# Optimization experiments

Measured on AMD Instinct MI355X. Metric: run time of the kernel, lower is better.

Reference implementation:

```python
import jax, jax.numpy as jnp
import numpy as np

B, S, D, H = 1, 2048, 768, 12
HD = D // H


def layer_norm(x, g, b, eps=1e-5):
    mu = x.mean(-1, keepdims=True)
    var = ((x - mu) ** 2).mean(-1, keepdims=True)
    return (x - mu) * jax.lax.rsqrt(var + eps) * g + b


def setup_inputs() -> dict:
    key = jax.random.key(0)
    ks = jax.random.split(key, 16)
    s = 0.02
    exp_encodings = jax.random.normal(ks[0], (B, S, D), dtype=jnp.float32)
    pert_encodings = jax.random.normal(ks[1], (B, S, D), dtype=jnp.float32)
    adj = (jax.random.uniform(ks[2], (S, S)) < 0.01).astype(jnp.int32)
    adj = adj.at[jnp.arange(S), jnp.arange(S)].set(1)
    in_proj_w = jax.random.normal(ks[3], (3 * D, D)) * s
    in_proj_b = jnp.zeros((3 * D,), jnp.float32)
    out_proj_w = jax.random.normal(ks[4], (D, D)) * s
    out_proj_b = jnp.zeros((D,), jnp.float32)
    ln0_g = jnp.ones((D,), jnp.float32); ln0_b = jnp.zeros((D,), jnp.float32)
    ln1_g = jnp.ones((D,), jnp.float32); ln1_b = jnp.zeros((D,), jnp.float32)
    ln2_g = jnp.ones((D,), jnp.float32); ln2_b = jnp.zeros((D,), jnp.float32)
    w1 = jax.random.normal(ks[5], (D // 2, D)) * s
    b1 = jnp.zeros((D // 2,), jnp.float32)
    w2 = jax.random.normal(ks[6], (D, D // 2)) * s
    b2 = jnp.zeros((D,), jnp.float32)
    return dict(exp_encodings=exp_encodings, pert_encodings=pert_encodings,
                in_proj_w=in_proj_w, in_proj_b=in_proj_b,
                out_proj_w=out_proj_w, out_proj_b=out_proj_b,
                ln0_g=ln0_g, ln0_b=ln0_b, ln1_g=ln1_g, ln1_b=ln1_b,
                ln2_g=ln2_g, ln2_b=ln2_b, w1=w1, b1=b1, w2=w2, b2=b2,
                adj=adj)


def reference(exp_encodings, pert_encodings, in_proj_w, in_proj_b,
              out_proj_w, out_proj_b, ln0_g, ln0_b, ln1_g, ln1_b,
              ln2_g, ln2_b, w1, b1, w2, b2, adj):
    b, s, d = exp_encodings.shape
    hd = d // H
    # additive mask: 0 where edge, -inf elsewhere (diag guaranteed edge)
    mask = jnp.where(adj > 0, 0.0, -jnp.inf).astype(exp_encodings.dtype)
    x_in = layer_norm(exp_encodings + pert_encodings, ln0_g, ln0_b)
    # torch MultiheadAttention (batch_first) self-attention
    qkv = x_in @ in_proj_w.T + in_proj_b          # [b,s,3d]
    q, k, v = jnp.split(qkv, 3, axis=-1)
    q = q.reshape(b, s, H, hd)
    k = k.reshape(b, s, H, hd)
    v = v.reshape(b, s, H, hd)
    scores = jnp.einsum('bqhe,bkhe->bhqk', q, k) / np.sqrt(hd) + mask
    attn = jax.nn.softmax(scores, axis=-1)
    o = jnp.einsum('bhqk,bkhe->bqhe', attn, v).reshape(b, s, d)
    o = o @ out_proj_w.T + out_proj_b
    x = layer_norm(o + x_in, ln1_g, ln1_b)
    ff = jax.nn.relu(x @ w1.T + b1) @ w2.T + b2
    return layer_norm(x + ff, ln2_g, ln2_b)
```

## Files before the change

kernel.cpp:

```cpp
#include <hip/hip_runtime.h>

#define S 2048
#define D 768
#define NH 12
#define HD 64
#define TD (3 * D)

typedef __bf16 bf16_t;
typedef __bf16 v8bf __attribute__((ext_vector_type(8)));
typedef __bf16 v4bf __attribute__((ext_vector_type(4)));
typedef float v4f __attribute__((ext_vector_type(4)));

__device__ __forceinline__ float wave_reduce_sum(float v) {
#pragma unroll
    for (int o = 32; o > 0; o >>= 1) v += __shfl_down(v, o, 64);
    return v;
}
__device__ float block_reduce_sum(float v) {
    __shared__ float t4[4];
    int lane = threadIdx.x & 63, wid = threadIdx.x >> 6;
    v = wave_reduce_sum(v);
    __syncthreads();
    if (lane == 0) t4[wid] = v;
    __syncthreads();
    return t4[0] + t4[1] + t4[2] + t4[3];
}

template <int N>
__device__ __forceinline__ void wait_vmcnt() {
    if constexpr (N == 0) asm volatile("s_waitcnt vmcnt(0)" ::: "memory");
    else if constexpr (N == 1) asm volatile("s_waitcnt vmcnt(1)" ::: "memory");
    else if constexpr (N == 2) asm volatile("s_waitcnt vmcnt(2)" ::: "memory");
    else if constexpr (N == 3) asm volatile("s_waitcnt vmcnt(3)" ::: "memory");
    else if constexpr (N == 4) asm volatile("s_waitcnt vmcnt(4)" ::: "memory");
    else if constexpr (N == 5) asm volatile("s_waitcnt vmcnt(5)" ::: "memory");
    else if constexpr (N == 6) asm volatile("s_waitcnt vmcnt(6)" ::: "memory");
    else if constexpr (N == 7) asm volatile("s_waitcnt vmcnt(7)" ::: "memory");
    else asm volatile("s_waitcnt vmcnt(8)" ::: "memory");
}

#define NW0 (TD * D / 4)
#define NW1 (D * D / 4)
#define NW2 ((D / 2) * D / 4)
#define NW3 (D * (D / 2) / 4)
#define NWALL (NW0 + NW1 + NW2 + NW3)

__global__ __launch_bounds__(256) void addln_cvt(const float* __restrict__ A, const float* __restrict__ Bv,
                                                 const float* __restrict__ g, const float* __restrict__ be,
                                                 bf16_t* __restrict__ out,
                                                 const float* __restrict__ s0, const float* __restrict__ s1,
                                                 const float* __restrict__ s2, const float* __restrict__ s3,
                                                 bf16_t* __restrict__ d0, bf16_t* __restrict__ d1,
                                                 bf16_t* __restrict__ d2, bf16_t* __restrict__ d3) {
    int blk = blockIdx.x, t = threadIdx.x;
    if (blk >= S) {
        int i = (blk - S) * 256 + t;
        const float* sp; bf16_t* dp;
        if (i < NW0) { sp = s0; dp = d0; }
        else if (i < NW0 + NW1) { sp = s1; dp = d1; i -= NW0; }
        else if (i < NW0 + NW1 + NW2) { sp = s2; dp = d2; i -= NW0 + NW1; }
        else if (i < NWALL) { sp = s3; dp = d3; i -= NW0 + NW1 + NW2; }
        else return;
        float4 v = ((const float4*)sp)[i];
        v4bf o = {(bf16_t)v.x, (bf16_t)v.y, (bf16_t)v.z, (bf16_t)v.w};
        *(v4bf*)(dp + (size_t)i * 4) = o;
        return;
    }
    int row = blk;
    const float* a = A + (size_t)row * D;
    const float* b = Bv + (size_t)row * D;
    float x[3];
    float s = 0.f;
#pragma unroll
    for (int i = 0; i < 3; ++i) { int c = t + 256 * i; x[i] = a[c] + b[c]; s += x[i]; }
    float mean = block_reduce_sum(s) * (1.0f / D);
    float vs = 0.f;
#pragma unroll
    for (int i = 0; i < 3; ++i) { float d = x[i] - mean; vs += d * d; }
    float var = block_reduce_sum(vs) * (1.0f / D);
    float rstd = rsqrtf(var + 1e-5f);
#pragma unroll
    for (int i = 0; i < 3; ++i) {
        int c = t + 256 * i;
        out[(size_t)row * D + c] = (bf16_t)((x[i] - mean) * rstd * g[c] + be[c]);
    }
}

template <typename TO>
__global__ __launch_bounds__(256) void ln_only(const bf16_t* __restrict__ X,
                                               const float* __restrict__ g, const float* __restrict__ be,
                                               TO* __restrict__ out) {
    int row = blockIdx.x, t = threadIdx.x;
    const bf16_t* a = X + (size_t)row * D;
    float x[3];
    float s = 0.f;
#pragma unroll
    for (int i = 0; i < 3; ++i) { int c = t + 256 * i; x[i] = (float)a[c]; s += x[i]; }
    float mean = block_reduce_sum(s) * (1.0f / D);
    float vs = 0.f;
#pragma unroll
    for (int i = 0; i < 3; ++i) { float d = x[i] - mean; vs += d * d; }
    float var = block_reduce_sum(vs) * (1.0f / D);
    float rstd = rsqrtf(var + 1e-5f);
#pragma unroll
    for (int i = 0; i < 3; ++i) {
        int c = t + 256 * i;
        out[(size_t)row * D + c] = (TO)((x[i] - mean) * rstd * g[c] + be[c]);
    }
}

#define GBK 64

template <int TM, int TN, int RELU, bool RESID>
__global__ __launch_bounds__(256) void gemm_mfma(const bf16_t* __restrict__ A, const bf16_t* __restrict__ B,
                                                 const float* __restrict__ bias,
                                                 const bf16_t* __restrict__ Rsd, bf16_t* __restrict__ C,
                                                 int M, int N, int K) {
    constexpr int CA = TM * 8;
    constexpr int CHUNKS = (TM + TN) * 8;
    constexpr int P = CHUNKS / 256;
    static_assert(CHUNKS % 256 == 0, "chunk passes must be exact");
    constexpr int MI = TM / 32, NI = TN / 32;
    constexpr int BUFE = (TM + TN) * GBK;
    __shared__ bf16_t smem[2 * BUFE];
    const int t = threadIdx.x;
    const int lane = t & 63, wave = t >> 6;
    const int wr = (wave >> 1) * (TM / 2), wc = (wave & 1) * (TN / 2);
    const int m0 = blockIdx.y * TM, n0 = blockIdx.x * TN;
    const int lm = lane & 15, q = lane >> 4;

    const bf16_t* gp[P];
    int loff[P];
#pragma unroll
    for (int p = 0; p < P; ++p) {
        int c = t + 256 * p;
        if (c < CA) {
            int slab = c / (TM * 4), r4 = c % (TM * 4);
            gp[p] = A + (size_t)(m0 + (r4 >> 2)) * K + slab * 32 + (r4 & 3) * 8;
            loff[p] = slab * (TM * 32) + r4 * 8;
        } else {
            int cc = c - CA;
            int slab = cc / (TN * 4), r4 = cc % (TN * 4);
            gp[p] = B + (size_t)(n0 + (r4 >> 2)) * K + slab * 32 + (r4 & 3) * 8;
            loff[p] = TM * GBK + slab * (TN * 32) + r4 * 8;
        }
    }

    v4f acc[MI][NI] = {};

    auto stage = [&](int buf, int k0) {
#pragma unroll
        for (int p = 0; p < P; ++p)
            __builtin_amdgcn_global_load_lds(
                (const __attribute__((address_space(1))) void*)(gp[p] + k0),
                (__attribute__((address_space(3))) void*)(smem + buf * BUFE + loff[p]), 16, 0, 0);
    };

    stage(0, 0);
    int cur = 0;
    for (int k0 = 0; k0 < K; k0 += GBK) {
        if (k0 + GBK < K) {
            stage(cur ^ 1, k0 + GBK);
            __builtin_amdgcn_sched_barrier(0);
            wait_vmcnt<P>();
        } else {
            __builtin_amdgcn_sched_barrier(0);
            wait_vmcnt<0>();
        }
        __builtin_amdgcn_s_barrier();
        __builtin_amdgcn_sched_barrier(0);

        const bf16_t* As = smem + cur * BUFE;
        const bf16_t* Bs = As + TM * GBK;
        v8bf af[2][MI], bfr[2][NI];
#pragma unroll
        for (int s = 0; s < 2; ++s) {
#pragma unroll
            for (int i = 0; i < MI; ++i)
                af[s][i] = *(const v8bf*)(As + s * (TM * 32) + (wr + i * 16 + lm) * 32 + q * 8);
#pragma unroll
            for (int j = 0; j < NI; ++j)
                bfr[s][j] = *(const v8bf*)(Bs + s * (TN * 32) + (wc + j * 16 + lm) * 32 + q * 8);
        }
#pragma unroll
        for (int s = 0; s < 2; ++s)
#pragma unroll
            for (int i = 0; i < MI; ++i)
#pragma unroll
                for (int j = 0; j < NI; ++j)
                    acc[i][j] = __builtin_amdgcn_mfma_f32_16x16x32_bf16(af[s][i], bfr[s][j], acc[i][j], 0, 0, 0);
        __builtin_amdgcn_sched_barrier(0);
        __builtin_amdgcn_s_barrier();
        cur ^= 1;
    }

#pragma unroll
    for (int i = 0; i < MI; ++i)
#pragma unroll
        for (int j = 0; j < NI; ++j) {
            int col = n0 + wc + j * 16 + lm;
            float bs = bias[col];
#pragma unroll
            for (int r = 0; r < 4; ++r) {
                int row = m0 + wr + i * 16 + q * 4 + r;
                float v = acc[i][j][r] + bs;
                if (RELU) v = fmaxf(v, 0.f);
                if (RESID) v += (float)Rsd[(size_t)row * N + col];
                C[(size_t)row * N + col] = (bf16_t)v;
            }
        }
}

__global__ __launch_bounds__(256) void attn_sparse(const bf16_t* __restrict__ qkv, const int* __restrict__ adj,
                                                   bf16_t* __restrict__ O) {
    __shared__ int s_idx[128];
    __shared__ int s_cnt;
    __shared__ float s_q[D];
    __shared__ float s_p[NH][128];

    const int row = blockIdx.x, t = threadIdx.x;
    const int lane = t & 63, wave = t >> 6;
    if (t == 0) s_cnt = 0;
    __syncthreads();

    const int4* arow = (const int4*)(adj + (size_t)row * S);
#pragma unroll
    for (int p = 0; p < 2; ++p) {
        int4 v = arow[t + 256 * p];
        int base = (t + 256 * p) * 4;
        if (v.x) { int k = atomicAdd(&s_cnt, 1); if (k < 128) s_idx[k] = base + 0; }
        if (v.y) { int k = atomicAdd(&s_cnt, 1); if (k < 128) s_idx[k] = base + 1; }
        if (v.z) { int k = atomicAdd(&s_cnt, 1); if (k < 128) s_idx[k] = base + 2; }
        if (v.w) { int k = atomicAdd(&s_cnt, 1); if (k < 128) s_idx[k] = base + 3; }
    }
    for (int c = t; c < D; c += 256) s_q[c] = (float)qkv[(size_t)row * TD + c];
    __syncthreads();
    const int n = (s_cnt < 128) ? s_cnt : 128;

    for (int it = t; it < n * NH; it += 256) {
        int h = it / n, i = it - h * n;
        int j = s_idx[i];
        const bf16_t* kp = qkv + (size_t)j * TD + D + h * HD;
        const float* qp = s_q + h * HD;
        float dot = 0.f;
#pragma unroll
        for (int c = 0; c < HD; c += 8) {
            v8bf kv = *(const v8bf*)(kp + c);
#pragma unroll
            for (int e = 0; e < 8; ++e) dot += qp[c + e] * (float)kv[e];
        }
        s_p[h][i] = dot * 0.125f;
    }
    __syncthreads();

    for (int h = wave; h < NH; h += 4) {
        float v0 = (lane < n) ? s_p[h][lane] : -1e30f;
        float v1 = (lane + 64 < n) ? s_p[h][lane + 64] : -1e30f;
        float m = fmaxf(v0, v1);
#pragma unroll
        for (int o = 32; o > 0; o >>= 1) m = fmaxf(m, __shfl_xor(m, o, 64));
        float p0 = (lane < n) ? __expf(v0 - m) : 0.f;
        float p1 = (lane + 64 < n) ? __expf(v1 - m) : 0.f;
        float sm = p0 + p1;
#pragma unroll
        for (int o = 32; o > 0; o >>= 1) sm += __shfl_xor(sm, o, 64);
        float inv = 1.f / sm;
        if (lane < n) s_p[h][lane] = p0 * inv;
        if (lane + 64 < n) s_p[h][lane + 64] = p1 * inv;
    }
    __syncthreads();

    for (int o = t; o < D; o += 256) {
        int h = o >> 6, e = o & 63;
        const float* pp = s_p[h];
        float acc = 0.f;
        for (int i = 0; i < n; ++i)
            acc += pp[i] * (float)qkv[(size_t)s_idx[i] * TD + 2 * D + h * HD + e];
        O[(size_t)row * D + o] = (bf16_t)acc;
    }
}

extern "C" void kernel_launch(void* const* d_in, const int* in_sizes, int n_in,
                              void* d_out, int out_size, void* d_ws, size_t ws_size,
                              hipStream_t stream) {
    const float* exp_e = (const float*)d_in[0];
    const float* pert  = (const float*)d_in[1];
    const float* w_in  = (const float*)d_in[2];
    const float* b_in  = (const float*)d_in[3];
    const float* w_out = (const float*)d_in[4];
    const float* b_out = (const float*)d_in[5];
    const float* g0  = (const float*)d_in[6];
    const float* be0 = (const float*)d_in[7];
    const float* g1  = (const float*)d_in[8];
    const float* be1 = (const float*)d_in[9];
    const float* g2  = (const float*)d_in[10];
    const float* be2 = (const float*)d_in[11];
    const float* w1  = (const float*)d_in[12];
    const float* b1  = (const float*)d_in[13];
    const float* w2  = (const float*)d_in[14];
    const float* b2  = (const float*)d_in[15];
    const int*   adj = (const int*)d_in[16];
    float* out = (float*)d_out;

    const size_t SD = (size_t)S * D;
    bf16_t* wb_in  = (bf16_t*)d_ws;
    bf16_t* wb_out = wb_in + (size_t)TD * D;
    bf16_t* wb_1   = wb_out + (size_t)D * D;
    bf16_t* wb_2   = wb_1 + (size_t)(D / 2) * D;
    bf16_t* x_in   = wb_2 + (size_t)D * (D / 2);
    bf16_t* qkv    = x_in + SD;
    bf16_t* attn_o = qkv + 3 * SD;
    bf16_t* y1     = attn_o + SD;
    bf16_t* x1     = y1 + SD;
    bf16_t* ffh    = x1 + SD;
    bf16_t* y2     = ffh + SD / 2;

    const int CVTB = (NWALL + 255) / 256;
    addln_cvt<<<S + CVTB, 256, 0, stream>>>(exp_e, pert, g0, be0, x_in,
                                            w_in, w_out, w1, w2, wb_in, wb_out, wb_1, wb_2);
    gemm_mfma<64, 128, 0, false><<<dim3(TD / 128, S / 64), 256, 0, stream>>>(x_in, wb_in, b_in, nullptr, qkv, S, TD, D);
    attn_sparse<<<S, 256, 0, stream>>>(qkv, adj, attn_o);
    gemm_mfma<64, 64, 0, true><<<dim3(D / 64, S / 64), 256, 0, stream>>>(attn_o, wb_out, b_out, x_in, y1, S, D, D);
    ln_only<bf16_t><<<S, 256, 0, stream>>>(y1, g1, be1, x1);
    gemm_mfma<32, 64, 1, false><<<dim3((D / 2) / 64, S / 32), 256, 0, stream>>>(x1, wb_1, b1, nullptr, ffh, S, D / 2, D);
    gemm_mfma<64, 64, 0, true><<<dim3(D / 64, S / 64), 256, 0, stream>>>(ffh, wb_2, b2, x1, y2, S, D, D / 2);
    ln_only<float><<<S, 256, 0, stream>>>(y2, g2, be2, out);
}
```

Baseline: 188.7 us.

## Fuse all stages into one persistent megakernel with software grid barriers

Replaces the eight separate launches with a single persistent kernel that loops over work units per stage and separates stages with a global atomic grid barrier. It also retiles the QKV GEMM to 128x96, rewrites sparse attention to one wave per row using ballot-based index compaction, and has each lane accumulate all heads in the PV loop. The aim is to remove launch gaps and tail effects between small kernels. In exchange, the grid barrier relies on every block being co-resident (grid size picked from an occupancy query) and risks deadlock, and the GEMMs run with fewer blocks than tiles.

```diff
diff --git a/kernel.cpp b/kernel.cpp
--- a/kernel.cpp
+++ b/kernel.cpp
@@ -5,11 +5,49 @@
 #define NH 12
 #define HD 64
 #define TD (3 * D)
+#define GBK 64
 
 typedef __bf16 bf16_t;
 typedef __bf16 v8bf __attribute__((ext_vector_type(8)));
 typedef __bf16 v4bf __attribute__((ext_vector_type(4)));
 typedef float v4f __attribute__((ext_vector_type(4)));
+
+#define NW0 (TD * D / 4)
+#define NW1 (D * D / 4)
+#define NW2 ((D / 2) * D / 4)
+#define NW3 (D * (D / 2) / 4)
+#define NWALL (NW0 + NW1 + NW2 + NW3)
+#define CVTB (NWALL / 256)
+
+union SMemU {
+    bf16_t g[2 * (128 + 96) * GBK];
+    struct {
+        int idx[4][128];
+        float q[4][D];
+        float p[4][NH * 128];
+    } at;
+};
+
+__device__ unsigned g_cnt = 0;
+__device__ unsigned g_gen = 0;
+
+__device__ __forceinline__ void grid_sync(int nb) {
+    __syncthreads();
+    if (threadIdx.x == 0) {
+        __threadfence();
+        unsigned g = __hip_atomic_load(&g_gen, __ATOMIC_RELAXED, __HIP_MEMORY_SCOPE_AGENT);
+        unsigned a = __hip_atomic_fetch_add(&g_cnt, 1u, __ATOMIC_ACQ_REL, __HIP_MEMORY_SCOPE_AGENT) + 1;
+        if (a == (unsigned)nb) {
+            __hip_atomic_store(&g_cnt, 0u, __ATOMIC_RELAXED, __HIP_MEMORY_SCOPE_AGENT);
+            __hip_atomic_fetch_add(&g_gen, 1u, __ATOMIC_RELEASE, __HIP_MEMORY_SCOPE_AGENT);
+        } else {
+            while (__hip_atomic_load(&g_gen, __ATOMIC_ACQUIRE, __HIP_MEMORY_SCOPE_AGENT) == g)
+                __builtin_amdgcn_s_sleep(2);
+        }
+        __threadfence();
+    }
+    __syncthreads();
+}
 
 __device__ __forceinline__ float wave_reduce_sum(float v) {
 #pragma unroll
@@ -39,34 +77,9 @@
     else asm volatile("s_waitcnt vmcnt(8)" ::: "memory");
 }
 
-#define NW0 (TD * D / 4)
-#define NW1 (D * D / 4)
-#define NW2 ((D / 2) * D / 4)
-#define NW3 (D * (D / 2) / 4)
-#define NWALL (NW0 + NW1 + NW2 + NW3)
-
-__global__ __launch_bounds__(256) void addln_cvt(const float* __restrict__ A, const float* __restrict__ Bv,
-                                                 const float* __restrict__ g, const float* __restrict__ be,
-                                                 bf16_t* __restrict__ out,
-                                                 const float* __restrict__ s0, const float* __restrict__ s1,
-                                                 const float* __restrict__ s2, const float* __restrict__ s3,
-                                                 bf16_t* __restrict__ d0, bf16_t* __restrict__ d1,
-                                                 bf16_t* __restrict__ d2, bf16_t* __restrict__ d3) {
-    int blk = blockIdx.x, t = threadIdx.x;
-    if (blk >= S) {
-        int i = (blk - S) * 256 + t;
-        const float* sp; bf16_t* dp;
-        if (i < NW0) { sp = s0; dp = d0; }
-        else if (i < NW0 + NW1) { sp = s1; dp = d1; i -= NW0; }
-        else if (i < NW0 + NW1 + NW2) { sp = s2; dp = d2; i -= NW0 + NW1; }
-        else if (i < NWALL) { sp = s3; dp = d3; i -= NW0 + NW1 + NW2; }
-        else return;
-        float4 v = ((const float4*)sp)[i];
-        v4bf o = {(bf16_t)v.x, (bf16_t)v.y, (bf16_t)v.z, (bf16_t)v.w};
-        *(v4bf*)(dp + (size_t)i * 4) = o;
-        return;
-    }
-    int row = blk;
+__device__ void addln_row(int row, int t, const float* __restrict__ A, const float* __restrict__ Bv,
+                          const float* __restrict__ g, const float* __restrict__ be,
+                          bf16_t* __restrict__ out) {
     const float* a = A + (size_t)row * D;
     const float* b = Bv + (size_t)row * D;
     float x[3];
@@ -87,10 +100,8 @@
 }
 
 template <typename TO>
-__global__ __launch_bounds__(256) void ln_only(const bf16_t* __restrict__ X,
-                                               const float* __restrict__ g, const float* __restrict__ be,
-                                               TO* __restrict__ out) {
-    int row = blockIdx.x, t = threadIdx.x;
+__device__ void ln_row(int row, int t, const bf16_t* __restrict__ X,
+                       const float* __restrict__ g, const float* __restrict__ be, TO* __restrict__ out) {
     const bf16_t* a = X + (size_t)row * D;
     float x[3];
     float s = 0.f;
@@ -109,24 +120,38 @@
     }
 }
 
-#define GBK 64
+__device__ void cvt_chunk(int ci, int t,
+                          const float* __restrict__ s0, const float* __restrict__ s1,
+                          const float* __restrict__ s2, const float* __restrict__ s3,
+                          bf16_t* __restrict__ d0, bf16_t* __restrict__ d1,
+                          bf16_t* __restrict__ d2, bf16_t* __restrict__ d3) {
+    int i = ci * 256 + t;
+    const float* sp; bf16_t* dp;
+    if (i < NW0) { sp = s0; dp = d0; }
+    else if (i < NW0 + NW1) { sp = s1; dp = d1; i -= NW0; }
+    else if (i < NW0 + NW1 + NW2) { sp = s2; dp = d2; i -= NW0 + NW1; }
+    else if (i < NWALL) { sp = s3; dp = d3; i -= NW0 + NW1 + NW2; }
+    else return;
+    float4 v = ((const float4*)sp)[i];
+    v4bf o = {(bf16_t)v.x, (bf16_t)v.y, (bf16_t)v.z, (bf16_t)v.w};
+    *(v4bf*)(dp + (size_t)i * 4) = o;
+}
 
 template <int TM, int TN, int RELU, bool RESID>
-__global__ __launch_bounds__(256) void gemm_mfma(const bf16_t* __restrict__ A, const bf16_t* __restrict__ B,
-                                                 const float* __restrict__ bias,
-                                                 const bf16_t* __restrict__ Rsd, bf16_t* __restrict__ C,
-                                                 int M, int N, int K) {
+__device__ void gemm_tile(bf16_t* __restrict__ smem, int bx, int by,
+                          const bf16_t* __restrict__ A, const bf16_t* __restrict__ B,
+                          const float* __restrict__ bias, const bf16_t* __restrict__ Rsd,
+                          bf16_t* __restrict__ C, int M, int N, int K) {
     constexpr int CA = TM * 8;
     constexpr int CHUNKS = (TM + TN) * 8;
     constexpr int P = CHUNKS / 256;
     static_assert(CHUNKS % 256 == 0, "chunk passes must be exact");
     constexpr int MI = TM / 32, NI = TN / 32;
     constexpr int BUFE = (TM + TN) * GBK;
-    __shared__ bf16_t smem[2 * BUFE];
     const int t = threadIdx.x;
     const int lane = t & 63, wave = t >> 6;
     const int wr = (wave >> 1) * (TM / 2), wc = (wave & 1) * (TN / 2);
-    const int m0 = blockIdx.y * TM, n0 = blockIdx.x * TN;
+    const int m0 = by * TM, n0 = bx * TN;
     const int lm = lane & 15, q = lane >> 4;
 
     const bf16_t* gp[P];
@@ -211,37 +236,40 @@
         }
 }
 
-__global__ __launch_bounds__(256) void attn_sparse(const bf16_t* __restrict__ qkv, const int* __restrict__ adj,
-                                                   bf16_t* __restrict__ O) {
-    __shared__ int s_idx[128];
-    __shared__ int s_cnt;
-    __shared__ float s_q[D];
-    __shared__ float s_p[NH][128];
-
-    const int row = blockIdx.x, t = threadIdx.x;
-    const int lane = t & 63, wave = t >> 6;
-    if (t == 0) s_cnt = 0;
-    __syncthreads();
-
+__device__ void attn_row(int row, int lane, const bf16_t* __restrict__ qkv, const int* __restrict__ adj,
+                         bf16_t* __restrict__ O, int* __restrict__ widx,
+                         float* __restrict__ wq, float* __restrict__ wp) {
+    int cnt = 0;
     const int4* arow = (const int4*)(adj + (size_t)row * S);
-#pragma unroll
-    for (int p = 0; p < 2; ++p) {
-        int4 v = arow[t + 256 * p];
-        int base = (t + 256 * p) * 4;
-        if (v.x) { int k = atomicAdd(&s_cnt, 1); if (k < 128) s_idx[k] = base + 0; }
-        if (v.y) { int k = atomicAdd(&s_cnt, 1); if (k < 128) s_idx[k] = base + 1; }
-        if (v.z) { int k = atomicAdd(&s_cnt, 1); if (k < 128) s_idx[k] = base + 2; }
-        if (v.w) { int k = atomicAdd(&s_cnt, 1); if (k < 128) s_idx[k] = base + 3; }
-    }
-    for (int c = t; c < D; c += 256) s_q[c] = (float)qkv[(size_t)row * TD + c];
-    __syncthreads();
-    const int n = (s_cnt < 128) ? s_cnt : 128;
-
-    for (int it = t; it < n * NH; it += 256) {
+    const unsigned long long lt = (1ull << lane) - 1;
+#pragma unroll
+    for (int p = 0; p < 8; ++p) {
+        int4 v = arow[lane + 64 * p];
+        int base = (lane + 64 * p) * 4;
+        int f[4] = {v.x, v.y, v.z, v.w};
+#pragma unroll
+        for (int c = 0; c < 4; ++c) {
+            unsigned long long m = __ballot(f[c] != 0);
+            if (f[c]) {
+                int k = cnt + (int)__popcll(m & lt);
+                if (k < 128) widx[k] = base + c;
+            }
+            cnt += (int)__popcll(m);
+        }
+    }
+    const int n = (cnt < 128) ? cnt : 128;
+
+    for (int ch = lane; ch < D / 8; ch += 64) {
+        v8bf qv = *(const v8bf*)(qkv + (size_t)row * TD + ch * 8);
+#pragma unroll
+        for (int e = 0; e < 8; ++e) wq[ch * 8 + e] = (float)qv[e];
+    }
+    __syncthreads();
+
+    for (int it = lane; it < n * NH; it += 64) {
         int h = it / n, i = it - h * n;
-        int j = s_idx[i];
-        const bf16_t* kp = qkv + (size_t)j * TD + D + h * HD;
-        const float* qp = s_q + h * HD;
+        const bf16_t* kp = qkv + (size_t)widx[i] * TD + D + h * HD;
+        const float* qp = wq + h * HD;
         float dot = 0.f;
 #pragma unroll
         for (int c = 0; c < HD; c += 8) {
@@ -249,13 +277,13 @@
 #pragma unroll
             for (int e = 0; e < 8; ++e) dot += qp[c + e] * (float)kv[e];
         }
-        s_p[h][i] = dot * 0.125f;
-    }
-    __syncthreads();
-
-    for (int h = wave; h < NH; h += 4) {
-        float v0 = (lane < n) ? s_p[h][lane] : -1e30f;
-        float v1 = (lane + 64 < n) ? s_p[h][lane + 64] : -1e30f;
+        wp[h * 128 + i] = dot * 0.125f;
+    }
+    __syncthreads();
+
+    for (int h = 0; h < NH; ++h) {
+        float v0 = (lane < n) ? wp[h * 128 + lane] : -1e30f;
+        float v1 = (lane + 64 < n) ? wp[h * 128 + lane + 64] : -1e30f;
         float m = fmaxf(v0, v1);
 #pragma unroll
         for (int o = 32; o > 0; o >>= 1) m = fmaxf(m, __shfl_xor(m, o, 64));
@@ -265,43 +293,71 @@
 #pragma unroll
         for (int o = 32; o > 0; o >>= 1) sm += __shfl_xor(sm, o, 64);
         float inv = 1.f / sm;
-        if (lane < n) s_p[h][lane] = p0 * inv;
-        if (lane + 64 < n) s_p[h][lane + 64] = p1 * inv;
-    }
-    __syncthreads();
-
-    for (int o = t; o < D; o += 256) {
-        int h = o >> 6, e = o & 63;
-        const float* pp = s_p[h];
-        float acc = 0.f;
-        for (int i = 0; i < n; ++i)
-            acc += pp[i] * (float)qkv[(size_t)s_idx[i] * TD + 2 * D + h * HD + e];
-        O[(size_t)row * D + o] = (bf16_t)acc;
-    }
+        if (lane < n) wp[h * 128 + lane] = p0 * inv;
+        if (lane + 64 < n) wp[h * 128 + lane + 64] = p1 * inv;
+    }
+    __syncthreads();
+
+    float acc[NH] = {};
+    for (int i = 0; i < n; ++i) {
+        const bf16_t* vp = qkv + (size_t)widx[i] * TD + 2 * D + lane;
+#pragma unroll
+        for (int j = 0; j < NH; ++j) acc[j] += wp[j * 128 + i] * (float)vp[j * HD];
+    }
+#pragma unroll
+    for (int j = 0; j < NH; ++j) O[(size_t)row * D + j * HD + lane] = (bf16_t)acc[j];
+}
+
+struct KArgs {
+    const float *exp_e, *pert, *w_in, *b_in, *w_out, *b_out;
+    const float *g0, *be0, *g1, *be1, *g2, *be2;
+    const float *w1, *b1, *w2, *b2;
+    const int* adj;
+    float* out;
+    bf16_t *wb_in, *wb_out, *wb_1, *wb_2;
+    bf16_t *x_in, *qkv, *attn_o, *y1, *x1, *ffh, *y2;
+};
+
+__global__ __launch_bounds__(256, 2) void mega(KArgs a, int nb) {
+    __shared__ SMemU sm;
+    const int blk = blockIdx.x, t = threadIdx.x;
+    const int lane = t & 63, wave = t >> 6;
+
+    for (int u = blk; u < S + CVTB; u += nb) {
+        if (u < S) addln_row(u, t, a.exp_e, a.pert, a.g0, a.be0, a.x_in);
+        else cvt_chunk(u - S, t, a.w_in, a.w_out, a.w1, a.w2, a.wb_in, a.wb_out, a.wb_1, a.wb_2);
+    }
+    grid_sync(nb);
+
+    for (int tile = blk; tile < 384; tile += nb)
+        gemm_tile<128, 96, 0, false>(sm.g, tile % 24, tile / 24, a.x_in, a.wb_in, a.b_in, nullptr, a.qkv, S, TD, D);
+    grid_sync(nb);
+
+    for (int row = blk * 4 + wave; row < S; row += nb * 4)
+        attn_row(row, lane, a.qkv, a.adj, a.attn_o, sm.at.idx[wave], sm.at.q[wave], sm.at.p[wave]);
+    grid_sync(nb);
+
+    for (int tile = blk; tile < 384; tile += nb)
+        gemm_tile<64, 64, 0, true>(sm.g, tile % 12, tile / 12, a.attn_o, a.wb_out, a.b_out, a.x_in, a.y1, S, D, D);
+    grid_sync(nb);
+
+    for (int u = blk; u < S; u += nb) ln_row<bf16_t>(u, t, a.y1, a.g1, a.be1, a.x1);
+    grid_sync(nb);
+
+    for (int tile = blk; tile < 384; tile += nb)
+        gemm_tile<32, 64, 1, false>(sm.g, tile % 6, tile / 6, a.x1, a.wb_1, a.b1, nullptr, a.ffh, S, D / 2, D);
+    grid_sync(nb);
+
+    for (int tile = blk; tile < 384; tile += nb)
+        gemm_tile<64, 64, 0, true>(sm.g, tile % 12, tile / 12, a.ffh, a.wb_2, a.b2, a.x1, a.y2, S, D, D / 2);
+    grid_sync(nb);
+
+    for (int u = blk; u < S; u += nb) ln_row<float>(u, t, a.y2, a.g2, a.be2, a.out);
 }
 
 extern "C" void kernel_launch(void* const* d_in, const int* in_sizes, int n_in,
                               void* d_out, int out_size, void* d_ws, size_t ws_size,
                               hipStream_t stream) {
-    const float* exp_e = (const float*)d_in[0];
-    const float* pert  = (const float*)d_in[1];
-    const float* w_in  = (const float*)d_in[2];
-    const float* b_in  = (const float*)d_in[3];
-    const float* w_out = (const float*)d_in[4];
-    const float* b_out = (const float*)d_in[5];
-    const float* g0  = (const float*)d_in[6];
-    const float* be0 = (const float*)d_in[7];
-    const float* g1  = (const float*)d_in[8];
-    const float* be1 = (const float*)d_in[9];
-    const float* g2  = (const float*)d_in[10];
-    const float* be2 = (const float*)d_in[11];
-    const float* w1  = (const float*)d_in[12];
-    const float* b1  = (const float*)d_in[13];
-    const float* w2  = (const float*)d_in[14];
-    const float* b2  = (const float*)d_in[15];
-    const int*   adj = (const int*)d_in[16];
-    float* out = (float*)d_out;
-
     const size_t SD = (size_t)S * D;
     bf16_t* wb_in  = (bf16_t*)d_ws;
     bf16_t* wb_out = wb_in + (size_t)TD * D;
@@ -315,14 +371,33 @@
     bf16_t* ffh    = x1 + SD;
     bf16_t* y2     = ffh + SD / 2;
 
-    const int CVTB = (NWALL + 255) / 256;
-    addln_cvt<<<S + CVTB, 256, 0, stream>>>(exp_e, pert, g0, be0, x_in,
-                                            w_in, w_out, w1, w2, wb_in, wb_out, wb_1, wb_2);
-    gemm_mfma<64, 128, 0, false><<<dim3(TD / 128, S / 64), 256, 0, stream>>>(x_in, wb_in, b_in, nullptr, qkv, S, TD, D);
-    attn_sparse<<<S, 256, 0, stream>>>(qkv, adj, attn_o);
-    gemm_mfma<64, 64, 0, true><<<dim3(D / 64, S / 64), 256, 0, stream>>>(attn_o, wb_out, b_out, x_in, y1, S, D, D);
-    ln_only<bf16_t><<<S, 256, 0, stream>>>(y1, g1, be1, x1);
-    gemm_mfma<32, 64, 1, false><<<dim3((D / 2) / 64, S / 32), 256, 0, stream>>>(x1, wb_1, b1, nullptr, ffh, S, D / 2, D);
-    gemm_mfma<64, 64, 0, true><<<dim3(D / 64, S / 64), 256, 0, stream>>>(ffh, wb_2, b2, x1, y2, S, D, D / 2);
-    ln_only<float><<<S, 256, 0, stream>>>(y2, g2, be2, out);
-}
+    KArgs a;
+    a.exp_e = (const float*)d_in[0];
+    a.pert  = (const float*)d_in[1];
+    a.w_in  = (const float*)d_in[2];
+    a.b_in  = (const float*)d_in[3];
+    a.w_out = (const float*)d_in[4];
+    a.b_out = (const float*)d_in[5];
+    a.g0  = (const float*)d_in[6];
+    a.be0 = (const float*)d_in[7];
+    a.g1  = (const float*)d_in[8];
+    a.be1 = (const float*)d_in[9];
+    a.g2  = (const float*)d_in[10];
+    a.be2 = (const float*)d_in[11];
+    a.w1  = (const float*)d_in[12];
+    a.b1  = (const float*)d_in[13];
+    a.w2  = (const float*)d_in[14];
+    a.b2  = (const float*)d_in[15];
+    a.adj = (const int*)d_in[16];
+    a.out = (float*)d_out;
+    a.wb_in = wb_in; a.wb_out = wb_out; a.wb_1 = wb_1; a.wb_2 = wb_2;
+    a.x_in = x_in; a.qkv = qkv; a.attn_o = attn_o; a.y1 = y1; a.x1 = x1; a.ffh = ffh; a.y2 = y2;
+
+    static int nb_cache = 0;
+    if (nb_cache == 0) {
+        int occ = 0;
+        hipError_t e = hipOccupancyMaxActiveBlocksPerMultiprocessor(&occ, mega, 256, 0);
+        nb_cache = (e == hipSuccess && occ >= 2) ? 512 : 256;
+    }
+    mega<<<nb_cache, 256, 0, stream>>>(a, nb_cache);
+}
```

Result: slower. 599.0 us (+217.4%).
